# Kernel optimization log

Hardware: AMD Instinct MI355X
Metric: run time of the kernel (lower is better)

Reference implementation:

```python
import jax, jax.numpy as jnp
import numpy as np

H = 1152
NH = 16
HD = H // NH
CTX = 768
MLP = int(H * 4.0)
EPS = 1e-6


def _ln(x):
    mu = jnp.mean(x, axis=-1, keepdims=True)
    var = jnp.mean(jnp.square(x - mu), axis=-1, keepdims=True)
    return (x - mu) / jnp.sqrt(var + EPS)


def _modulate(x, shift, scale):
    return x * (1 + scale[:, None, :]) + shift[:, None, :]


def _gelu_tanh(x):
    c = jnp.float32(np.sqrt(2.0 / np.pi))
    return 0.5 * x * (1.0 + jnp.tanh(c * (x + 0.044715 * x * x * x)))


def _heads(t, nh):
    B, N, C = t.shape
    return t.reshape(B, N, nh, C // nh).transpose(0, 2, 1, 3)  # [B,h,N,hd]


def setup_inputs() -> dict:
    key = jax.random.key(0)
    ks = jax.random.split(key, 20)
    s = lambda fan_in: 1.0 / np.sqrt(fan_in)
    d = {
        'x': jax.random.normal(ks[0], (8, 1024, H), jnp.float32),
        'c': jax.random.normal(ks[1], (8, 77, CTX), jnp.float32),
        't_emb': jax.random.normal(ks[2], (8, H), jnp.float32),
        'qkv_w': jax.random.normal(ks[3], (3 * H, H), jnp.float32) * s(H),
        'qkv_b': jnp.zeros((3 * H,), jnp.float32),
        'proj_w': jax.random.normal(ks[4], (H, H), jnp.float32) * s(H),
        'proj_b': jnp.zeros((H,), jnp.float32),
        'to_q_w': jax.random.normal(ks[5], (H, H), jnp.float32) * s(H),
        'to_k_w': jax.random.normal(ks[6], (H, CTX), jnp.float32) * s(CTX),
        'to_v_w': jax.random.normal(ks[7], (H, CTX), jnp.float32) * s(CTX),
        'to_out_w': jax.random.normal(ks[8], (H, H), jnp.float32) * s(H),
        'to_out_b': jnp.zeros((H,), jnp.float32),
        'mlp_w1': jax.random.normal(ks[9], (MLP, H), jnp.float32) * s(H),
        'mlp_b1': jnp.zeros((MLP,), jnp.float32),
        'mlp_w2': jax.random.normal(ks[10], (H, MLP), jnp.float32) * s(MLP),
        'mlp_b2': jnp.zeros((H,), jnp.float32),
        'ada_w': jax.random.normal(ks[11], (6 * H, H), jnp.float32) * s(H),
        'ada_b': jnp.zeros((6 * H,), jnp.float32),
    }
    return d


def reference(x, c, t_emb, qkv_w, qkv_b, proj_w, proj_b, to_q_w, to_k_w, to_v_w,
              to_out_w, to_out_b, mlp_w1, mlp_b1, mlp_w2, mlp_b2, ada_w, ada_b):
    B, N, C = x.shape
    scale = HD ** -0.5

    # adaLN modulation
    mod = jax.nn.silu(t_emb) @ ada_w.T + ada_b  # [B,6H]
    sh_msa, sc_msa, g_msa, sh_mlp, sc_mlp, g_mlp = jnp.split(mod, 6, axis=1)

    # self-attention
    h = _modulate(_ln(x), sh_msa, sc_msa)
    qkv = h @ qkv_w.T + qkv_b  # [B,N,3H]
    q, k, v = jnp.split(qkv, 3, axis=-1)
    q, k, v = _heads(q, NH), _heads(k, NH), _heads(v, NH)
    attn = jax.nn.softmax(jnp.einsum('bhnd,bhmd->bhnm', q, k) * scale, axis=-1)
    o = jnp.einsum('bhnm,bhmd->bhnd', attn, v).transpose(0, 2, 1, 3).reshape(B, N, C)
    x = x + g_msa[:, None, :] * (o @ proj_w.T + proj_b)

    # cross-attention
    q = _heads(x @ to_q_w.T, NH)
    k = _heads(c @ to_k_w.T, NH)
    v = _heads(c @ to_v_w.T, NH)
    attn = jax.nn.softmax(jnp.einsum('bhnd,bhmd->bhnm', q, k) * scale, axis=-1)
    o = jnp.einsum('bhnm,bhmd->bhnd', attn, v).transpose(0, 2, 1, 3).reshape(B, N, C)
    x = x + (o @ to_out_w.T + to_out_b)

    # gated MLP
    h = _modulate(_ln(x), sh_mlp, sc_mlp)
    h = _gelu_tanh(h @ mlp_w1.T + mlp_b1) @ mlp_w2.T + mlp_b2
    return x + g_mlp[:, None, :] * h
```

## Files before the change

kernel.cpp:

```cpp
#include <hip/hip_runtime.h>
#include <stdint.h>

typedef __bf16 bf16;
typedef bf16 bf16x8 __attribute__((ext_vector_type(8)));
typedef bf16 bf16x4 __attribute__((ext_vector_type(4)));
typedef float f32x4 __attribute__((ext_vector_type(4)));

#define DEV __device__ __forceinline__


DEV void gload_lds16(const bf16* g, bf16* l) {
  __builtin_amdgcn_global_load_lds((const __attribute__((address_space(1))) void*)g,
                                   (__attribute__((address_space(3))) void*)l,
                                   16, 0, 0);
}

DEV uint32_t pkbf(float a, float b) {
  unsigned short ua = __builtin_bit_cast(unsigned short, (bf16)a);
  unsigned short ub = __builtin_bit_cast(unsigned short, (bf16)b);
  return (uint32_t)ua | ((uint32_t)ub << 16);
}

union U8 { uint32_t u[4]; bf16x8 v; };


__global__ void f2b_kernel(const float* __restrict__ in, bf16* __restrict__ out, int n4) {
  int i = blockIdx.x * 256 + threadIdx.x;
  if (i < n4) {
    float4 v = ((const float4*)in)[i];
    bf16x4 o;
    o[0] = (bf16)v.x; o[1] = (bf16)v.y; o[2] = (bf16)v.z; o[3] = (bf16)v.w;
    *(bf16x4*)(out + (size_t)i * 4) = o;
  }
}


__global__ void silu_kernel(const float* __restrict__ in, float* __restrict__ out, int n) {
  int i = blockIdx.x * 256 + threadIdx.x;
  if (i < n) { float v = in[i]; out[i] = v / (1.0f + __expf(-v)); }
}


__global__ __launch_bounds__(256) void mod_kernel(
    const float* __restrict__ st, const float* __restrict__ ada_w,
    const float* __restrict__ ada_b, float* __restrict__ modout) {
  int gw = (blockIdx.x * 256 + threadIdx.x) >> 6;
  int lane = threadIdx.x & 63;
  if (gw >= 8 * 6912) return;
  int b = gw / 6912, j = gw % 6912;
  const float* sp = st + b * 1152;
  const float* wp = ada_w + (size_t)j * 1152;
  float acc = 0.f;
  for (int k = lane; k < 1152; k += 64) acc += sp[k] * wp[k];
  #pragma unroll
  for (int off = 32; off; off >>= 1) acc += __shfl_xor(acc, off);
  if (lane == 0) modout[(size_t)b * 6912 + j] = acc + ada_b[j];
}


__global__ __launch_bounds__(256) void ln_mod_kernel(
    const float* __restrict__ x, const float* __restrict__ mod,
    int sh_off, int sc_off, bf16* __restrict__ out) {
  int row = blockIdx.x, tid = threadIdx.x;
  int b = row >> 10;
  const float* xr = x + (size_t)row * 1152;
  float vals[5];
  float s = 0.f, s2 = 0.f;
  #pragma unroll
  for (int it = 0; it < 5; ++it) {
    int i = tid + it * 256;
    float v = (i < 1152) ? xr[i] : 0.f;
    vals[it] = v; s += v; s2 += v * v;
  }
  #pragma unroll
  for (int off = 32; off; off >>= 1) { s += __shfl_xor(s, off); s2 += __shfl_xor(s2, off); }
  __shared__ float rs[4], rs2[4];
  int w = tid >> 6, lane = tid & 63;
  if (lane == 0) { rs[w] = s; rs2[w] = s2; }
  __syncthreads();
  s = rs[0] + rs[1] + rs[2] + rs[3];
  s2 = rs2[0] + rs2[1] + rs2[2] + rs2[3];
  float mu = s * (1.0f / 1152.0f);
  float var = s2 * (1.0f / 1152.0f) - mu * mu;
  float rstd = rsqrtf(var + 1e-6f);
  const float* shp = mod + (size_t)b * 6912 + sh_off;
  const float* scp = mod + (size_t)b * 6912 + sc_off;
  #pragma unroll
  for (int it = 0; it < 5; ++it) {
    int i = tid + it * 256;
    if (i < 1152) {
      float v = (vals[it] - mu) * rstd;
      out[(size_t)row * 1152 + i] = (bf16)(v * (1.0f + scp[i]) + shp[i]);
    }
  }
}


DEV void stage_tile(const bf16* src, int ld, int row0, int maxrow, int k0,
                    bf16* lds, int tid) {
  int lane = tid & 63, wv = tid >> 6;
  #pragma unroll
  for (int j = 0; j < 2; ++j) {
    int r = j * 64 + wv * 16 + (lane >> 2);
    int kk = (lane & 3) * 8;
    int gr = min(row0 + r, maxrow);
    const bf16* g = src + (size_t)gr * ld + k0 + kk;
    bf16* l = lds + (j * 64 + wv * 16) * 32;
    gload_lds16(g, l);
  }
}

template <int EP>
__global__ __launch_bounds__(256) void gemm_bt(
    const bf16* __restrict__ A, int lda,
    const bf16* __restrict__ W, int ldw,
    const float* __restrict__ bias,
    bf16* __restrict__ Cb, int ldc,
    float* __restrict__ Cf,
    const float* __restrict__ resid,
    const float* __restrict__ gate, int gate_off,
    bf16* __restrict__ Cb2,
    int M, int N, int K) {
  __shared__ __align__(16) bf16 lA[128 * 32];
  __shared__ __align__(16) bf16 lB[128 * 32];
  int tid = threadIdx.x, lane = tid & 63, w = tid >> 6;
  int wr = w >> 1, wc = w & 1;
  int row0 = blockIdx.x * 128, col0 = blockIdx.y * 128;
  f32x4 acc[4][4] = {};
  int nk = K >> 5;
  int rbase = wr * 64 + (lane & 15);
  int cbase = wc * 64 + (lane & 15);
  int koff = (lane >> 4) * 8;
  for (int ks = 0; ks < nk; ++ks) {
    stage_tile(A, lda, row0, M - 1, ks * 32, lA, tid);
    stage_tile(W, ldw, col0, N - 1, ks * 32, lB, tid);
    __syncthreads();
    bf16x8 af[4], bg[4];
    #pragma unroll
    for (int i = 0; i < 4; ++i) af[i] = *(const bf16x8*)&lA[(rbase + i * 16) * 32 + koff];
    #pragma unroll
    for (int i = 0; i < 4; ++i) bg[i] = *(const bf16x8*)&lB[(cbase + i * 16) * 32 + koff];
    #pragma unroll
    for (int mi = 0; mi < 4; ++mi)
      #pragma unroll
      for (int ni = 0; ni < 4; ++ni)
        acc[mi][ni] = __builtin_amdgcn_mfma_f32_16x16x32_bf16(af[mi], bg[ni], acc[mi][ni], 0, 0, 0);
    __syncthreads();
  }
  int r0 = row0 + wr * 64, c0 = col0 + wc * 64;
  #pragma unroll
  for (int mi = 0; mi < 4; ++mi)
    #pragma unroll
    for (int ni = 0; ni < 4; ++ni)
      #pragma unroll
      for (int rg = 0; rg < 4; ++rg) {
        int r = r0 + mi * 16 + (lane >> 4) * 4 + rg;
        int cc = c0 + ni * 16 + (lane & 15);
        if (r < M) {
          float v = acc[mi][ni][rg];
          if (bias) v += bias[cc];
          if constexpr (EP == 0) {
            Cb[(size_t)r * ldc + cc] = (bf16)v;
          } else if constexpr (EP == 1) {
            float gt = gate ? gate[(size_t)(r >> 10) * 6912 + gate_off + cc] : 1.0f;
            float o = resid[(size_t)r * ldc + cc] + gt * v;
            Cf[(size_t)r * ldc + cc] = o;
            if (Cb2) Cb2[(size_t)r * ldc + cc] = (bf16)o;
          } else {
            float t = tanhf(0.7978845608028654f * (v + 0.044715f * v * v * v));
            Cb[(size_t)r * ldc + cc] = (bf16)(0.5f * v * (1.0f + t));
          }
        }
      }
}


__global__ __launch_bounds__(256) void attn_kernel(
    const bf16* __restrict__ Q, long q_b, int q_h_off, int q_ld,
    const bf16* __restrict__ K, long k_b, int k_h_off, int k_ld,
    const bf16* __restrict__ V, long v_b, int v_h_off, int v_ld,
    bf16* __restrict__ O, long o_b, int o_h_off, int o_ld,
    int Nk, float scale) {
  __shared__ __align__(16) bf16 lK[32 * 104];
  __shared__ __align__(16) bf16 lVT[80 * 40];
  int tid = threadIdx.x, lane = tid & 63, w = tid >> 6;
  int bz = blockIdx.z, hy = blockIdx.y;
  int q0 = blockIdx.x * 256;
  int g = lane >> 4, i16 = lane & 15;
  const bf16* Qb = Q + (long)bz * q_b + (long)hy * q_h_off;
  const bf16* Kb = K + (long)bz * k_b + (long)hy * k_h_off;
  const bf16* Vb = V + (long)bz * v_b + (long)hy * v_h_off;

  bf16x8 qf[4][3];
  #pragma unroll
  for (int qp = 0; qp < 4; ++qp) {
    const bf16* qrow = Qb + (long)(q0 + w * 64 + qp * 16 + i16) * q_ld;
    qf[qp][0] = *(const bf16x8*)(qrow + g * 8);
    qf[qp][1] = *(const bf16x8*)(qrow + 32 + g * 8);
    if (g == 0) qf[qp][2] = *(const bf16x8*)(qrow + 64);
    else { bf16x8 z = {}; qf[qp][2] = z; }
  }

  for (int i = tid; i < 512; i += 256) {
    int r = i >> 4, cu = i & 15;
    ((uint32_t*)lK)[r * 52 + 36 + cu] = 0;
  }

  float m[4], l[4];
  #pragma unroll
  for (int qp = 0; qp < 4; ++qp) { m[qp] = -1e30f; l[qp] = 0.f; }
  f32x4 ot[5][4] = {};

  for (int k0 = 0; k0 < Nk; k0 += 32) {
    __syncthreads();
    #pragma unroll
    for (int s = 0; s < 2; ++s) {
      int cidx = tid + s * 256;
      if (cidx < 288) {
        int r = cidx & 31, cch = cidx >> 5;
        int krow = k0 + r;
        uint4 val = {0, 0, 0, 0};
        if (krow < Nk) val = *(const uint4*)(Kb + (long)krow * k_ld + cch * 8);
        *(uint4*)&lK[r * 104 + cch * 8] = val;
      }
    }
    #pragma unroll
    for (int s = 0; s < 2; ++s) {
      int cidx = tid + s * 256;
      if (cidx < 288) {
        int r = cidx & 31, cch = cidx >> 5;
        int vrow = k0 + r;
        uint4 val = {0, 0, 0, 0};
        if (vrow < Nk) val = *(const uint4*)(Vb + (long)vrow * v_ld + cch * 8);
        uint32_t uu[4] = {val.x, val.y, val.z, val.w};
        #pragma unroll
        for (int j = 0; j < 4; ++j) {
          lVT[(cch * 8 + 2 * j) * 40 + r]     = __builtin_bit_cast(bf16, (unsigned short)(uu[j] & 0xffffu));
          lVT[(cch * 8 + 2 * j + 1) * 40 + r] = __builtin_bit_cast(bf16, (unsigned short)(uu[j] >> 16));
        }
      }
    }
    __syncthreads();

    bf16x8 ka[3], kb[3];
    #pragma unroll
    for (int cD = 0; cD < 3; ++cD) {
      ka[cD] = *(const bf16x8*)&lK[i16 * 104 + cD * 32 + g * 8];
      kb[cD] = *(const bf16x8*)&lK[(16 + i16) * 104 + cD * 32 + g * 8];
    }

    bf16x8 pu[4];
    #pragma unroll
    for (int qp = 0; qp < 4; ++qp) {
      f32x4 sa = {}, sb = {};
      #pragma unroll
      for (int cD = 0; cD < 3; ++cD) {
        sa = __builtin_amdgcn_mfma_f32_16x16x32_bf16(ka[cD], qf[qp][cD], sa, 0, 0, 0);
        sb = __builtin_amdgcn_mfma_f32_16x16x32_bf16(kb[cD], qf[qp][cD], sb, 0, 0, 0);
      }
      float p[8];
      #pragma unroll
      for (int r = 0; r < 4; ++r) { p[r] = sa[r] * scale; p[4 + r] = sb[r] * scale; }
      if (k0 + 32 > Nk) {
        #pragma unroll
        for (int r = 0; r < 4; ++r) {
          if (k0 + g * 4 + r >= Nk)      p[r]     = -1e30f;
          if (k0 + 16 + g * 4 + r >= Nk) p[4 + r] = -1e30f;
        }
      }
      float tm = p[0];
      #pragma unroll
      for (int j = 1; j < 8; ++j) tm = fmaxf(tm, p[j]);
      tm = fmaxf(tm, __shfl_xor(tm, 16));
      tm = fmaxf(tm, __shfl_xor(tm, 32));
      float mnew = fmaxf(m[qp], tm);
      float alpha = __expf(m[qp] - mnew);
      float psum = 0.f;
      #pragma unroll
      for (int j = 0; j < 8; ++j) { p[j] = __expf(p[j] - mnew); psum += p[j]; }
      psum += __shfl_xor(psum, 16);
      psum += __shfl_xor(psum, 32);
      l[qp] = l[qp] * alpha + psum;
      m[qp] = mnew;
      #pragma unroll
      for (int dt = 0; dt < 5; ++dt) ot[dt][qp] *= alpha;
      uint32_t dA0 = pkbf(p[0], p[1]), dA1 = pkbf(p[2], p[3]);
      uint32_t dB0 = pkbf(p[4], p[5]), dB1 = pkbf(p[6], p[7]);
      int s0 = ((2 * g) & 3) * 16 + i16;
      int s1 = s0 + 16;
      uint32_t wa0 = (uint32_t)__shfl((int)dA0, s0), wa1 = (uint32_t)__shfl((int)dA1, s0);
      uint32_t wa2 = (uint32_t)__shfl((int)dA0, s1), wa3 = (uint32_t)__shfl((int)dA1, s1);
      uint32_t wb0 = (uint32_t)__shfl((int)dB0, s0), wb1 = (uint32_t)__shfl((int)dB1, s0);
      uint32_t wb2 = (uint32_t)__shfl((int)dB0, s1), wb3 = (uint32_t)__shfl((int)dB1, s1);
      U8 puu;
      puu.u[0] = g < 2 ? wa0 : wb0;
      puu.u[1] = g < 2 ? wa1 : wb1;
      puu.u[2] = g < 2 ? wa2 : wb2;
      puu.u[3] = g < 2 ? wa3 : wb3;
      pu[qp] = puu.v;
    }
    #pragma unroll
    for (int dt = 0; dt < 5; ++dt) {
      bf16x8 vt = *(const bf16x8*)&lVT[(dt * 16 + i16) * 40 + g * 8];
      #pragma unroll
      for (int qp = 0; qp < 4; ++qp)
        ot[dt][qp] = __builtin_amdgcn_mfma_f32_16x16x32_bf16(vt, pu[qp], ot[dt][qp], 0, 0, 0);
    }
  }
  #pragma unroll
  for (int qp = 0; qp < 4; ++qp) {
    float inv = 1.0f / l[qp];
    bf16* orow = O + (long)bz * o_b + (long)hy * o_h_off +
                 (long)(q0 + w * 64 + qp * 16 + i16) * o_ld;
    #pragma unroll
    for (int dt = 0; dt < 5; ++dt)
      #pragma unroll
      for (int rg = 0; rg < 4; ++rg) {
        int d = dt * 16 + g * 4 + rg;
        if (d < 72) orow[d] = (bf16)(ot[dt][qp][rg] * inv);
      }
  }
}


extern "C" void kernel_launch(void* const* d_in, const int* in_sizes, int n_in,
                              void* d_out, int out_size, void* d_ws, size_t ws_size,
                              hipStream_t stream) {
  (void)in_sizes; (void)n_in; (void)out_size; (void)ws_size;
  const float* x        = (const float*)d_in[0];
  const float* c        = (const float*)d_in[1];
  const float* t_emb    = (const float*)d_in[2];
  const float* qkv_w    = (const float*)d_in[3];
  const float* qkv_b    = (const float*)d_in[4];
  const float* proj_w   = (const float*)d_in[5];
  const float* proj_b   = (const float*)d_in[6];
  const float* to_q_w   = (const float*)d_in[7];
  const float* to_k_w   = (const float*)d_in[8];
  const float* to_v_w   = (const float*)d_in[9];
  const float* to_out_w = (const float*)d_in[10];
  const float* to_out_b = (const float*)d_in[11];
  const float* mlp_w1   = (const float*)d_in[12];
  const float* mlp_b1   = (const float*)d_in[13];
  const float* mlp_w2   = (const float*)d_in[14];
  const float* mlp_b2   = (const float*)d_in[15];
  const float* ada_w    = (const float*)d_in[16];
  const float* ada_b    = (const float*)d_in[17];
  float* out = (float*)d_out;

  char* ws = (char*)d_ws;
  size_t off = 0;
  auto alloc = [&](size_t b) { size_t o = off; off += (b + 255) & ~(size_t)255; return o; };
  bf16* wq    = (bf16*)(ws + alloc((size_t)3456 * 1152 * 2));
  bf16* wproj = (bf16*)(ws + alloc((size_t)1152 * 1152 * 2));
  bf16* wtoq  = (bf16*)(ws + alloc((size_t)1152 * 1152 * 2));
  bf16* wtok  = (bf16*)(ws + alloc((size_t)1152 * 768 * 2));
  bf16* wtov  = (bf16*)(ws + alloc((size_t)1152 * 768 * 2));
  bf16* wtoout= (bf16*)(ws + alloc((size_t)1152 * 1152 * 2));
  bf16* wm1   = (bf16*)(ws + alloc((size_t)4608 * 1152 * 2));
  bf16* wm2   = (bf16*)(ws + alloc((size_t)1152 * 4608 * 2));
  bf16* cb    = (bf16*)(ws + alloc((size_t)616 * 768 * 2));
  float* stl  = (float*)(ws + alloc((size_t)8 * 1152 * 4));
  float* modb = (float*)(ws + alloc((size_t)8 * 6912 * 4));
  bf16* S1    = (bf16*)(ws + alloc((size_t)8192 * 1152 * 2));
  bf16* R1    = (bf16*)(ws + alloc((size_t)8192 * 4608 * 2));
  bf16* R2    = (bf16*)(ws + alloc((size_t)8192 * 1152 * 2));
  float* x2   = (float*)(ws + alloc((size_t)8192 * 1152 * 4));

  bf16* qkvbuf = R1;
  bf16* q2 = R1;
  bf16* kc = (bf16*)((char*)R1 + (size_t)8192 * 1152 * 2);
  bf16* vc = (bf16*)((char*)kc + (size_t)616 * 1152 * 2);
  bf16* mid = R1;

  auto cvt = [&](const float* src, bf16* dst, size_t n) {
    int n4 = (int)(n / 4);
    f2b_kernel<<<(n4 + 255) / 256, 256, 0, stream>>>(src, dst, n4);
  };
  cvt(qkv_w,    wq,    (size_t)3456 * 1152);
  cvt(proj_w,   wproj, (size_t)1152 * 1152);
  cvt(to_q_w,   wtoq,  (size_t)1152 * 1152);
  cvt(to_k_w,   wtok,  (size_t)1152 * 768);
  cvt(to_v_w,   wtov,  (size_t)1152 * 768);
  cvt(to_out_w, wtoout,(size_t)1152 * 1152);
  cvt(mlp_w1,   wm1,   (size_t)4608 * 1152);
  cvt(mlp_w2,   wm2,   (size_t)1152 * 4608);
  cvt(c,        cb,    (size_t)616 * 768);

  silu_kernel<<<36, 256, 0, stream>>>(t_emb, stl, 8 * 1152);
  mod_kernel<<<13824, 256, 0, stream>>>(stl, ada_w, ada_b, modb);

  ln_mod_kernel<<<8192, 256, 0, stream>>>(x, modb, 0, 1152, S1);

  gemm_bt<0><<<dim3(64, 27), 256, 0, stream>>>(S1, 1152, wq, 1152, qkv_b,
      qkvbuf, 3456, nullptr, nullptr, nullptr, 0, nullptr, 8192, 3456, 1152);

  const float scale = 0.11785113019775793f;
  attn_kernel<<<dim3(4, 16, 8), 256, 0, stream>>>(
      qkvbuf,        (long)1024 * 3456, 72, 3456,
      qkvbuf + 1152, (long)1024 * 3456, 72, 3456,
      qkvbuf + 2304, (long)1024 * 3456, 72, 3456,
      R2,            (long)1024 * 1152, 72, 1152,
      1024, scale);

  gemm_bt<1><<<dim3(64, 9), 256, 0, stream>>>(R2, 1152, wproj, 1152, proj_b,
      nullptr, 1152, x2, x, modb, 2304, S1, 8192, 1152, 1152);

  gemm_bt<0><<<dim3(64, 9), 256, 0, stream>>>(S1, 1152, wtoq, 1152, nullptr,
      q2, 1152, nullptr, nullptr, nullptr, 0, nullptr, 8192, 1152, 1152);
  gemm_bt<0><<<dim3(5, 9), 256, 0, stream>>>(cb, 768, wtok, 768, nullptr,
      kc, 1152, nullptr, nullptr, nullptr, 0, nullptr, 616, 1152, 768);
  gemm_bt<0><<<dim3(5, 9), 256, 0, stream>>>(cb, 768, wtov, 768, nullptr,
      vc, 1152, nullptr, nullptr, nullptr, 0, nullptr, 616, 1152, 768);

  attn_kernel<<<dim3(4, 16, 8), 256, 0, stream>>>(
      q2, (long)1024 * 1152, 72, 1152,
      kc, (long)77 * 1152,   72, 1152,
      vc, (long)77 * 1152,   72, 1152,
      R2, (long)1024 * 1152, 72, 1152,
      77, scale);

  gemm_bt<1><<<dim3(64, 9), 256, 0, stream>>>(R2, 1152, wtoout, 1152, to_out_b,
      nullptr, 1152, out, x2, nullptr, 0, nullptr, 8192, 1152, 1152);

  ln_mod_kernel<<<8192, 256, 0, stream>>>(out, modb, 3456, 4608, S1);

  gemm_bt<2><<<dim3(64, 36), 256, 0, stream>>>(S1, 1152, wm1, 1152, mlp_b1,
      mid, 4608, nullptr, nullptr, nullptr, 0, nullptr, 8192, 4608, 1152);

  gemm_bt<1><<<dim3(64, 9), 256, 0, stream>>>(mid, 4608, wm2, 4608, mlp_b2,
      nullptr, 1152, out, out, modb, 5760, nullptr, 8192, 1152, 4608);
}
```

Measured before the change: 1.260 ms.

## Double-buffer attention K/V tiles and use lazy exp2 softmax rescaling

The attention kernel now keeps two LDS buffers for K and transposed V. The next tile is prefetched into registers while the current one is computed, so there is one barrier per tile instead of two. Softmax switches to exp2 with log2e folded into the scale, and only rescales the running max and accumulators when the max grows past a threshold. The V transpose writes packed 32-bit words. This uses more LDS and registers and lets unnormalized probabilities grow larger before rescaling.

```diff
diff --git a/kernel.cpp b/kernel.cpp
--- a/kernel.cpp
+++ b/kernel.cpp
@@ -180,9 +180,10 @@
     const bf16* __restrict__ K, long k_b, int k_h_off, int k_ld,
     const bf16* __restrict__ V, long v_b, int v_h_off, int v_ld,
     bf16* __restrict__ O, long o_b, int o_h_off, int o_ld,
-    int Nk, float scale) {
-  __shared__ __align__(16) bf16 lK[32 * 104];
-  __shared__ __align__(16) bf16 lVT[80 * 40];
+    int Nk, float scale2) {
+  __shared__ __align__(16) bf16 lK[2][32 * 104];
+  __shared__ __align__(16) bf16 lVT[2][80 * 40];
+  const float THR = 11.5424f;
   int tid = threadIdx.x, lane = tid & 63, w = tid >> 6;
   int bz = blockIdx.z, hy = blockIdx.y;
   int q0 = blockIdx.x * 256;
@@ -201,52 +202,76 @@
     else { bf16x8 z = {}; qf[qp][2] = z; }
   }
 
-  for (int i = tid; i < 512; i += 256) {
-    int r = i >> 4, cu = i & 15;
-    ((uint32_t*)lK)[r * 52 + 36 + cu] = 0;
-  }
+  for (int i = tid; i < 1024; i += 256) {
+    int b = i >> 9, r = (i >> 4) & 31, cu = i & 15;
+    ((uint32_t*)lK[b])[r * 52 + 36 + cu] = 0;
+  }
+
+  int kr = tid & 31, kch = tid >> 5;
+  int vrp = tid & 15, vch = tid >> 4;
+
+  uint4 rk0, rk1, rv0, rv1;
+  int nt = (Nk + 31) >> 5;
+
+  {
+    int k0 = 0;
+    uint4 z = {0, 0, 0, 0};
+    rk0 = z; rk1 = z; rv0 = z; rv1 = z;
+    int krow = k0 + kr;
+    if (krow < Nk) rk0 = *(const uint4*)(Kb + (long)krow * k_ld + kch * 8);
+    if (tid < 32 && (k0 + tid) < Nk) rk1 = *(const uint4*)(Kb + (long)(k0 + tid) * k_ld + 64);
+    if (tid < 144) {
+      int r0 = k0 + 2 * vrp, r1 = r0 + 1;
+      if (r0 < Nk) rv0 = *(const uint4*)(Vb + (long)r0 * v_ld + vch * 8);
+      if (r1 < Nk) rv1 = *(const uint4*)(Vb + (long)r1 * v_ld + vch * 8);
+    }
+    *(uint4*)&lK[0][kr * 104 + kch * 8] = rk0;
+    if (tid < 32) *(uint4*)&lK[0][tid * 104 + 64] = rk1;
+    if (tid < 144) {
+      uint32_t a[4] = {rv0.x, rv0.y, rv0.z, rv0.w};
+      uint32_t b[4] = {rv1.x, rv1.y, rv1.z, rv1.w};
+      uint32_t* wv = (uint32_t*)&lVT[0][0];
+      #pragma unroll
+      for (int j = 0; j < 8; ++j) {
+        uint32_t lo = (a[j >> 1] >> ((j & 1) * 16)) & 0xffffu;
+        uint32_t hi = (b[j >> 1] >> ((j & 1) * 16)) & 0xffffu;
+        wv[(vch * 8 + j) * 20 + vrp] = lo | (hi << 16);
+      }
+    }
+  }
+  __syncthreads();
 
   float m[4], l[4];
   #pragma unroll
   for (int qp = 0; qp < 4; ++qp) { m[qp] = -1e30f; l[qp] = 0.f; }
   f32x4 ot[5][4] = {};
 
-  for (int k0 = 0; k0 < Nk; k0 += 32) {
-    __syncthreads();
-    #pragma unroll
-    for (int s = 0; s < 2; ++s) {
-      int cidx = tid + s * 256;
-      if (cidx < 288) {
-        int r = cidx & 31, cch = cidx >> 5;
-        int krow = k0 + r;
-        uint4 val = {0, 0, 0, 0};
-        if (krow < Nk) val = *(const uint4*)(Kb + (long)krow * k_ld + cch * 8);
-        *(uint4*)&lK[r * 104 + cch * 8] = val;
-      }
-    }
-    #pragma unroll
-    for (int s = 0; s < 2; ++s) {
-      int cidx = tid + s * 256;
-      if (cidx < 288) {
-        int r = cidx & 31, cch = cidx >> 5;
-        int vrow = k0 + r;
-        uint4 val = {0, 0, 0, 0};
-        if (vrow < Nk) val = *(const uint4*)(Vb + (long)vrow * v_ld + cch * 8);
-        uint32_t uu[4] = {val.x, val.y, val.z, val.w};
-        #pragma unroll
-        for (int j = 0; j < 4; ++j) {
-          lVT[(cch * 8 + 2 * j) * 40 + r]     = __builtin_bit_cast(bf16, (unsigned short)(uu[j] & 0xffffu));
-          lVT[(cch * 8 + 2 * j + 1) * 40 + r] = __builtin_bit_cast(bf16, (unsigned short)(uu[j] >> 16));
-        }
-      }
-    }
-    __syncthreads();
+  int cur = 0;
+  for (int t = 0; t < nt; ++t) {
+    int nxt = t + 1;
+    if (nxt < nt) {
+      int k0 = nxt * 32;
+      uint4 z = {0, 0, 0, 0};
+      rk0 = z; rk1 = z; rv0 = z; rv1 = z;
+      int krow = k0 + kr;
+      if (krow < Nk) rk0 = *(const uint4*)(Kb + (long)krow * k_ld + kch * 8);
+      if (tid < 32 && (k0 + tid) < Nk) rk1 = *(const uint4*)(Kb + (long)(k0 + tid) * k_ld + 64);
+      if (tid < 144) {
+        int r0 = k0 + 2 * vrp, r1 = r0 + 1;
+        if (r0 < Nk) rv0 = *(const uint4*)(Vb + (long)r0 * v_ld + vch * 8);
+        if (r1 < Nk) rv1 = *(const uint4*)(Vb + (long)r1 * v_ld + vch * 8);
+      }
+    }
+
+    const bf16* lKc = lK[cur];
+    const bf16* lVc = lVT[cur];
+    int k0 = t * 32;
 
     bf16x8 ka[3], kb[3];
     #pragma unroll
     for (int cD = 0; cD < 3; ++cD) {
-      ka[cD] = *(const bf16x8*)&lK[i16 * 104 + cD * 32 + g * 8];
-      kb[cD] = *(const bf16x8*)&lK[(16 + i16) * 104 + cD * 32 + g * 8];
+      ka[cD] = *(const bf16x8*)&lKc[i16 * 104 + cD * 32 + g * 8];
+      kb[cD] = *(const bf16x8*)&lKc[(16 + i16) * 104 + cD * 32 + g * 8];
     }
 
     bf16x8 pu[4];
@@ -260,7 +285,7 @@
       }
       float p[8];
       #pragma unroll
-      for (int r = 0; r < 4; ++r) { p[r] = sa[r] * scale; p[4 + r] = sb[r] * scale; }
+      for (int r = 0; r < 4; ++r) { p[r] = sa[r] * scale2; p[4 + r] = sb[r] * scale2; }
       if (k0 + 32 > Nk) {
         #pragma unroll
         for (int r = 0; r < 4; ++r) {
@@ -273,17 +298,20 @@
       for (int j = 1; j < 8; ++j) tm = fmaxf(tm, p[j]);
       tm = fmaxf(tm, __shfl_xor(tm, 16));
       tm = fmaxf(tm, __shfl_xor(tm, 32));
-      float mnew = fmaxf(m[qp], tm);
-      float alpha = __expf(m[qp] - mnew);
+      float dlt = tm - m[qp];
+      float alpha = 1.0f;
+      if (dlt > THR) { alpha = exp2f(-dlt); m[qp] = tm; }
+      float mq = m[qp];
       float psum = 0.f;
       #pragma unroll
-      for (int j = 0; j < 8; ++j) { p[j] = __expf(p[j] - mnew); psum += p[j]; }
+      for (int j = 0; j < 8; ++j) { p[j] = exp2f(p[j] - mq); psum += p[j]; }
       psum += __shfl_xor(psum, 16);
       psum += __shfl_xor(psum, 32);
       l[qp] = l[qp] * alpha + psum;
-      m[qp] = mnew;
-      #pragma unroll
-      for (int dt = 0; dt < 5; ++dt) ot[dt][qp] *= alpha;
+      if (__any(alpha != 1.0f)) {
+        #pragma unroll
+        for (int dt = 0; dt < 5; ++dt) ot[dt][qp] *= alpha;
+      }
       uint32_t dA0 = pkbf(p[0], p[1]), dA1 = pkbf(p[2], p[3]);
       uint32_t dB0 = pkbf(p[4], p[5]), dB1 = pkbf(p[6], p[7]);
       int s0 = ((2 * g) & 3) * 16 + i16;
@@ -301,12 +329,32 @@
     }
     #pragma unroll
     for (int dt = 0; dt < 5; ++dt) {
-      bf16x8 vt = *(const bf16x8*)&lVT[(dt * 16 + i16) * 40 + g * 8];
+      bf16x8 vt = *(const bf16x8*)&lVc[(dt * 16 + i16) * 40 + g * 8];
       #pragma unroll
       for (int qp = 0; qp < 4; ++qp)
         ot[dt][qp] = __builtin_amdgcn_mfma_f32_16x16x32_bf16(vt, pu[qp], ot[dt][qp], 0, 0, 0);
     }
-  }
+
+    if (nxt < nt) {
+      int nb = cur ^ 1;
+      *(uint4*)&lK[nb][kr * 104 + kch * 8] = rk0;
+      if (tid < 32) *(uint4*)&lK[nb][tid * 104 + 64] = rk1;
+      if (tid < 144) {
+        uint32_t a[4] = {rv0.x, rv0.y, rv0.z, rv0.w};
+        uint32_t b[4] = {rv1.x, rv1.y, rv1.z, rv1.w};
+        uint32_t* wv = (uint32_t*)&lVT[nb][0];
+        #pragma unroll
+        for (int j = 0; j < 8; ++j) {
+          uint32_t lo = (a[j >> 1] >> ((j & 1) * 16)) & 0xffffu;
+          uint32_t hi = (b[j >> 1] >> ((j & 1) * 16)) & 0xffffu;
+          wv[(vch * 8 + j) * 20 + vrp] = lo | (hi << 16);
+        }
+      }
+      __syncthreads();
+      cur = nb;
+    }
+  }
+
   #pragma unroll
   for (int qp = 0; qp < 4; ++qp) {
     float inv = 1.0f / l[qp];
@@ -394,13 +442,13 @@
   gemm_bt<0><<<dim3(64, 27), 256, 0, stream>>>(S1, 1152, wq, 1152, qkv_b,
       qkvbuf, 3456, nullptr, nullptr, nullptr, 0, nullptr, 8192, 3456, 1152);
 
-  const float scale = 0.11785113019775793f;
+  const float scale2 = 0.11785113019775793f * 1.4426950408889634f;
   attn_kernel<<<dim3(4, 16, 8), 256, 0, stream>>>(
       qkvbuf,        (long)1024 * 3456, 72, 3456,
       qkvbuf + 1152, (long)1024 * 3456, 72, 3456,
       qkvbuf + 2304, (long)1024 * 3456, 72, 3456,
       R2,            (long)1024 * 1152, 72, 1152,
-      1024, scale);
+      1024, scale2);
 
   gemm_bt<1><<<dim3(64, 9), 256, 0, stream>>>(R2, 1152, wproj, 1152, proj_b,
       nullptr, 1152, x2, x, modb, 2304, S1, 8192, 1152, 1152);
@@ -417,7 +465,7 @@
       kc, (long)77 * 1152,   72, 1152,
       vc, (long)77 * 1152,   72, 1152,
       R2, (long)1024 * 1152, 72, 1152,
-      77, scale);
+      77, scale2);
 
   gemm_bt<1><<<dim3(64, 9), 256, 0, stream>>>(R2, 1152, wtoout, 1152, to_out_b,
       nullptr, 1152, out, x2, nullptr, 0, nullptr, 8192, 1152, 1152);
```

After: 1.223 ms. 1.03x faster.
